# Kernel tuning notes

Measured on AMD Instinct MI355X. Metric: run time of the kernel, lower is better.

Reference implementation:

```python
import math
import jax, jax.numpy as jnp
import numpy as np
from jax import lax


def _l2n(v, eps=1e-12):
    return v / (jnp.linalg.norm(v) + eps)


def _sn(w_bar, u, v):
    # one power iteration (as in SpectralNorm with power_iterations=1)
    h = w_bar.shape[0]
    wm = w_bar.reshape(h, -1)
    v = _l2n(wm.T @ u)
    u = _l2n(wm @ v)
    u = lax.stop_gradient(u)  # u, v are updated via .data in torch (no grad)
    v = lax.stop_gradient(v)
    sigma = u @ (wm @ v)
    return w_bar / sigma


def _conv(x, w, stride, pad):
    return lax.conv_general_dilated(
        x, w, (stride, stride), [(pad, pad), (pad, pad)],
        dimension_numbers=('NCHW', 'OIHW', 'NCHW'))


def _make_blur_kernel():
    k = jnp.array([1., 3., 3., 1.], jnp.float32)
    k2 = k[None, :] * k[:, None]
    return k2 / k2.sum()  # 4x4, sums to 1


def _blur(x, k2, pad):
    # upfirdn2d with up=1, down=1: pad then depthwise FIR filter
    C = x.shape[1]
    xp = jnp.pad(x, ((0, 0), (0, 0), (pad[0], pad[1]), (pad[0], pad[1])))
    w = jnp.tile(k2[None, None], (C, 1, 1, 1))  # [C,1,4,4]
    return lax.conv_general_dilated(
        xp, w, (1, 1), 'VALID', feature_group_count=C,
        dimension_numbers=('NCHW', 'OIHW', 'NCHW'))


def setup_inputs() -> dict:
    key = jax.random.key(0)
    ks = jax.random.split(key, 12)
    Cin, Cout = 256, 512
    x = jax.random.normal(ks[0], (16, Cin, 64, 64), jnp.float32)
    w1_bar = jax.random.normal(ks[1], (Cin, Cin, 3, 3), jnp.float32) * 0.05
    u1 = _l2n(jax.random.normal(ks[2], (Cin,), jnp.float32))
    v1 = _l2n(jax.random.normal(ks[3], (Cin * 9,), jnp.float32))
    b1 = jnp.zeros((Cin,), jnp.float32)
    w2_bar = jax.random.normal(ks[4], (Cout, Cin, 3, 3), jnp.float32) * 0.05
    u2 = _l2n(jax.random.normal(ks[5], (Cout,), jnp.float32))
    v2 = _l2n(jax.random.normal(ks[6], (Cin * 9,), jnp.float32))
    b2 = jnp.zeros((Cout,), jnp.float32)
    ws_bar = jax.random.normal(ks[7], (Cout, Cin, 1, 1), jnp.float32) * 0.05
    us = _l2n(jax.random.normal(ks[8], (Cout,), jnp.float32))
    vs = _l2n(jax.random.normal(ks[9], (Cin,), jnp.float32))
    return dict(x=x, w1_bar=w1_bar, u1=u1, v1=v1, b1=b1,
                w2_bar=w2_bar, u2=u2, v2=v2, b2=b2,
                ws_bar=ws_bar, us=us, vs=vs)


def reference(x, w1_bar, u1, v1, b1, w2_bar, u2, v2, b2, ws_bar, us, vs):
    k2 = _make_blur_kernel()
    # conv1: 3x3 same-res, SN conv + bias + LeakyReLU(0.2)
    out = _conv(x, _sn(w1_bar, u1, v1), 1, 1) + b1[None, :, None, None]
    out = jax.nn.leaky_relu(out, 0.2)
    # conv2: blur pad=(2,2) then 3x3 stride-2 SN conv + bias + LeakyReLU
    out = _blur(out, k2, (2, 2))
    out = _conv(out, _sn(w2_bar, u2, v2), 2, 0) + b2[None, :, None, None]
    out = jax.nn.leaky_relu(out, 0.2)
    # skip: blur pad=(1,1) then 1x1 stride-2 SN conv (no bias, no act)
    skip = _blur(x, k2, (1, 1))
    skip = _conv(skip, _sn(ws_bar, us, vs), 2, 0)
    return (out + skip) / math.sqrt(2)
```

## Files before the change

### kernel.cpp

```cpp
#include <hip/hip_runtime.h>
#include <math.h>

typedef unsigned short u16;
typedef __attribute__((ext_vector_type(8))) unsigned short ushort8;
typedef __attribute__((ext_vector_type(4))) unsigned short u16x4;
typedef __attribute__((ext_vector_type(8))) short short8;
typedef __attribute__((ext_vector_type(4))) float f32x4;

__device__ __forceinline__ float b2f(u16 v) {
    unsigned u = ((unsigned)v) << 16; float f; __builtin_memcpy(&f, &u, 4); return f;
}
__device__ __forceinline__ u16 f2b(float f) {
    unsigned u; __builtin_memcpy(&u, &f, 4);
    u = (u + 0x7fffu + ((u >> 16) & 1u)) >> 16;
    return (u16)u;
}
__device__ __forceinline__ float ldin(const void* p, int i, int flag) {
    return flag ? ((const float*)p)[i] : b2f(((const u16*)p)[i]);
}
__device__ __forceinline__ void split2(float x, u16& h, u16& l) {
    h = f2b(x);
    l = f2b(x - b2f(h));
}
__device__ __forceinline__ ushort8 zero8() {
    ushort8 z;
#pragma unroll
    for (int i = 0; i < 8; ++i) z[i] = 0;
    return z;
}

__global__ void detect_kernel(const unsigned* __restrict__ xw, int* __restrict__ flag) {
    __shared__ int red[4];
    int tid = threadIdx.x, lane = tid & 63, wid = tid >> 6;
    int cnt = 0;
    for (int i = 0; i < 16; ++i) {
        unsigned w = xw[tid * 16 + i];
        unsigned e = (w >> 23) & 0xFF;
        if (e >= 77u && e <= 157u) ++cnt;
    }
    for (int o = 32; o; o >>= 1) cnt += __shfl_down(cnt, o, 64);
    if (lane == 0) red[wid] = cnt;
    __syncthreads();
    if (tid == 0) flag[0] = (red[0] + red[1] + red[2] + red[3] >= 2048) ? 1 : 0;
}

__global__ void sig_init_kernel(float* __restrict__ t, float* __restrict__ ns) {
    int i = blockIdx.x * 256 + threadIdx.x;
    if (i < 4864) t[i] = 0.f;
    if (i < 3) ns[i] = 0.f;
}

__global__ void sig_t_kernel(const void* __restrict__ w1, const void* __restrict__ u1,
                             const void* __restrict__ w2, const void* __restrict__ u2,
                             const void* __restrict__ wsb, const void* __restrict__ us,
                             const int* __restrict__ flagp, float* __restrict__ t) {
    __shared__ float ush[64];
    int blk = blockIdx.x;
    int flag = flagp[0];
    const void* W; const void* U; int m, toff, jc, ic;
    if (blk < 36)       { W = w1;  U = u1; m = 2304; toff = 0;    jc = blk % 9; ic = blk / 9; }
    else if (blk < 108) { int r = blk - 36;  W = w2;  U = u2; m = 2304; toff = 2304; jc = r % 9; ic = r / 9; }
    else                { int r = blk - 108; W = wsb; U = us; m = 256;  toff = 4608; jc = 0;     ic = r; }
    int tid = threadIdx.x;
    if (tid < 64) ush[tid] = ldin(U, ic * 64 + tid, flag);
    __syncthreads();
    int j = jc * 256 + tid;
    float acc = 0.f;
    int base = ic * 64 * m + j;
    for (int ii = 0; ii < 64; ++ii) acc += ldin(W, base + ii * m, flag) * ush[ii];
    atomicAdd(&t[toff + j], acc);
}

__global__ void sig_norm_kernel(float* __restrict__ t, float* __restrict__ ntinv) {
    __shared__ float red[4];
    int b = blockIdx.x;
    int m = (b == 2) ? 256 : 2304;
    int toff = b * 2304;
    int tid = threadIdx.x, lane = tid & 63, wid = tid >> 6;
    float s = 0.f;
    for (int j = tid; j < m; j += 256) { float v = t[toff + j]; s += v * v; }
    for (int o = 32; o; o >>= 1) s += __shfl_down(s, o, 64);
    if (lane == 0) red[wid] = s;
    __syncthreads();
    if (tid == 0) ntinv[b] = 1.f / (sqrtf(red[0] + red[1] + red[2] + red[3]) + 1e-12f);
}

__global__ void sig_s_kernel(const void* __restrict__ w1, const void* __restrict__ w2,
                             const void* __restrict__ wsb, const int* __restrict__ flagp,
                             const float* __restrict__ t, const float* __restrict__ ntinv,
                             float* __restrict__ ns) {
    int flag = flagp[0];
    int wg = blockIdx.x * 4 + (threadIdx.x >> 6);
    int lane = threadIdx.x & 63;
    const void* W; int m, toff, i, b;
    if (wg < 256)      { W = w1;  m = 2304; toff = 0;    i = wg;       b = 0; }
    else if (wg < 768) { W = w2;  m = 2304; toff = 2304; i = wg - 256; b = 1; }
    else               { W = wsb; m = 256;  toff = 4608; i = wg - 768; b = 2; }
    float acc = 0.f;
    int base = i * m;
    for (int j = lane; j < m; j += 64) acc += ldin(W, base + j, flag) * t[toff + j];
    for (int o = 32; o; o >>= 1) acc += __shfl_down(acc, o, 64);
    if (lane == 0) { float s = acc * ntinv[b]; atomicAdd(&ns[b], s * s); }
}

__global__ void sig_fin_kernel(const float* __restrict__ ns, float* __restrict__ inv_sigma) {
    int b = threadIdx.x;
    if (b < 3) { float s2 = ns[b]; float s = sqrtf(s2); inv_sigma[b] = (s + 1e-12f) / s2; }
}

__global__ void wprep_kernel(const void* __restrict__ w1b, const void* __restrict__ w2b,
                             const void* __restrict__ wsb,
                             const void* __restrict__ b1,  const void* __restrict__ b2,
                             const float* __restrict__ inv_sigma, const int* __restrict__ flagp,
                             u16* __restrict__ w1h, u16* __restrict__ w1l,
                             u16* __restrict__ w2h, u16* __restrict__ w2l,
                             u16* __restrict__ wsh, u16* __restrict__ wsl,
                             float* __restrict__ b1f, float* __restrict__ b2f_) {
    int idx = blockIdx.x * 256 + threadIdx.x;
    int flag = flagp[0];
    float s0 = inv_sigma[0], s1 = inv_sigma[1], s2 = inv_sigma[2];
    if (idx < 589824) {
        int kyx = idx / 65536; int rem = idx - kyx * 65536;
        int co = rem >> 8, ci = rem & 255;
        float w = ldin(w1b, ((co << 8) + ci) * 9 + kyx, flag) * s0;
        split2(w, w1h[idx], w1l[idx]);
    } else if (idx < 589824 + 1179648) {
        int i2 = idx - 589824;
        int kyx = i2 / 131072; int rem = i2 - kyx * 131072;
        int co = rem >> 8, ci = rem & 255;
        float w = ldin(w2b, ((co << 8) + ci) * 9 + kyx, flag) * s1;
        split2(w, w2h[i2], w2l[i2]);
    } else if (idx < 1900544) {
        int i3 = idx - 1769472;
        float w = ldin(wsb, i3, flag) * s2;
        split2(w, wsh[i3], wsl[i3]);
    } else if (idx < 1900544 + 256) {
        b1f[idx - 1900544] = ldin(b1, idx - 1900544, flag);
    } else if (idx < 1900544 + 768) {
        b2f_[idx - 1900800] = ldin(b2, idx - 1900800, flag);
    }
}

__global__ void transpose_kernel(const void* __restrict__ x, u16* __restrict__ xh,
                                 u16* __restrict__ xl,
                                 const int* __restrict__ flagp, int n0) {
    __shared__ float tile[32][65];
    int flag = flagp[0];
    int ny  = blockIdx.x;
    int ci0 = blockIdx.y * 32;
    int nl = ny >> 6, y = ny & 63;
    int t = threadIdx.x;
    int ci_l = t >> 3, x8 = (t & 7) * 8;
    int base = ((n0 + nl) * 256 + ci0 + ci_l) * 4096 + y * 64 + x8;
#pragma unroll
    for (int k = 0; k < 8; ++k) tile[ci_l][x8 + k] = ldin(x, base + k, flag);
    __syncthreads();
    int x_l = t >> 2, oc = (t & 3) * 8;
    size_t o = ((size_t)ny * 64 + x_l) * 256 + ci0 + oc;
    ushort8 h, l;
#pragma unroll
    for (int k = 0; k < 8; ++k) {
        u16 hh, ll; split2(tile[oc + k][x_l], hh, ll);
        h[k] = hh; l[k] = ll;
    }
    *(ushort8*)&xh[o] = h;
    *(ushort8*)&xl[o] = l;
}

__device__ __constant__ float BW[4] = {0.125f, 0.375f, 0.375f, 0.125f};

__global__ void blur1_kernel(const float* __restrict__ act1, u16* __restrict__ bh,
                             u16* __restrict__ bl) {
    int idx = blockIdx.x * 256 + threadIdx.x;
    int q = (idx & 63) * 4;
    int rem = idx >> 6;
    int xq = rem % 65; rem /= 65;
    int yq = rem % 65;
    int n  = rem / 65;
    float4 acc = {0.f, 0.f, 0.f, 0.f};
#pragma unroll
    for (int i = 0; i < 4; ++i) {
        int yy = yq + i - 2;
        if ((unsigned)yy >= 64u) continue;
#pragma unroll
        for (int j = 0; j < 4; ++j) {
            int xx = xq + j - 2;
            if ((unsigned)xx >= 64u) continue;
            float w = BW[i] * BW[j];
            float4 v = *(const float4*)&act1[((size_t)((n * 64 + yy) * 64 + xx) << 8) + q];
            acc.x += w * v.x; acc.y += w * v.y; acc.z += w * v.z; acc.w += w * v.w;
        }
    }
    u16x4 h, l;
    u16 hh, ll;
    split2(acc.x, hh, ll); h[0] = hh; l[0] = ll;
    split2(acc.y, hh, ll); h[1] = hh; l[1] = ll;
    split2(acc.z, hh, ll); h[2] = hh; l[2] = ll;
    split2(acc.w, hh, ll); h[3] = hh; l[3] = ll;
    *(u16x4*)&bh[(size_t)idx * 4] = h;
    *(u16x4*)&bl[(size_t)idx * 4] = l;
}

__global__ void blursample_kernel(const u16* __restrict__ xh, const u16* __restrict__ xl,
                                  u16* __restrict__ sh, u16* __restrict__ sl) {
    int idx = blockIdx.x * 256 + threadIdx.x;
    int q = (idx & 63) * 4;
    int rem = idx >> 6;
    int xo = rem & 31;
    int yo = (rem >> 5) & 31;
    int n  = rem >> 10;
    float4 acc = {0.f, 0.f, 0.f, 0.f};
#pragma unroll
    for (int i = 0; i < 4; ++i) {
        int yy = 2 * yo + i - 1;
        if ((unsigned)yy >= 64u) continue;
#pragma unroll
        for (int j = 0; j < 4; ++j) {
            int xx = 2 * xo + j - 1;
            if ((unsigned)xx >= 64u) continue;
            float w = BW[i] * BW[j];
            size_t g = ((size_t)((n * 64 + yy) * 64 + xx) << 8) + q;
            u16x4 vh = *(const u16x4*)&xh[g];
            u16x4 vl = *(const u16x4*)&xl[g];
            acc.x += w * (b2f(vh[0]) + b2f(vl[0]));
            acc.y += w * (b2f(vh[1]) + b2f(vl[1]));
            acc.z += w * (b2f(vh[2]) + b2f(vl[2]));
            acc.w += w * (b2f(vh[3]) + b2f(vl[3]));
        }
    }
    u16x4 h, l;
    u16 hh, ll;
    split2(acc.x, hh, ll); h[0] = hh; l[0] = ll;
    split2(acc.y, hh, ll); h[1] = hh; l[1] = ll;
    split2(acc.z, hh, ll); h[2] = hh; l[2] = ll;
    split2(acc.w, hh, ll); h[3] = hh; l[3] = ll;
    *(u16x4*)&sh[(size_t)idx * 4] = h;
    *(u16x4*)&sl[(size_t)idx * 4] = l;
}

#define LDK 40

template <bool DOLO>
__device__ __forceinline__ void conv1_body(
        const u16* __restrict__ xh, const u16* __restrict__ xl,
        const u16* __restrict__ w1h, const u16* __restrict__ w1l,
        const float* __restrict__ b1f, float* __restrict__ act1,
        u16* Ah, u16* Al, u16* Bh, u16* Bl) {
    int tid = threadIdx.x, lane = tid & 63, wid = tid >> 6;
    int col = lane & 15, quad = lane >> 4;
    int wco = (wid >> 1) * 32, wsp = (wid & 1) * 64;
    int sp_base = blockIdx.x * 128;
    int co_base = blockIdx.y * 64;
    int n  = sp_base >> 12;
    int y0 = (sp_base & 4095) >> 6;
    int r_st = tid >> 1, k_st = (tid & 1) * 16;
    int ra = tid >> 2, ka = (tid & 3) * 8;

    f32x4 acc[2][4];
#pragma unroll
    for (int i = 0; i < 2; ++i)
#pragma unroll
        for (int j = 0; j < 4; ++j) acc[i][j] = (f32x4){0.f, 0.f, 0.f, 0.f};

    for (int p = 0; p < 9; ++p) {
        int dy = p / 3 - 1, dx = p % 3 - 1;
        const u16* wh = w1h + (size_t)p * 65536;
        const u16* wl = w1l + (size_t)p * 65536;
        for (int kc = 0; kc < 8; ++kc) {
            int ci0 = kc * 32;
            __syncthreads();
            {
                size_t gs = (size_t)(co_base + ra) * 256 + ci0 + ka;
                *(ushort8*)&Ah[ra * LDK + ka] = *(const ushort8*)&wh[gs];
                if (DOLO) *(ushort8*)&Al[ra * LDK + ka] = *(const ushort8*)&wl[gs];
            }
            {
                int yy = y0 + (r_st >> 6) + dy;
                int xx = (r_st & 63) + dx;
                ushort8 h0, h1, l0, l1;
                if ((unsigned)yy < 64u && (unsigned)xx < 64u) {
                    size_t g = ((size_t)((n * 64 + yy) * 64 + xx) << 8) + ci0 + k_st;
                    h0 = *(const ushort8*)&xh[g];
                    h1 = *(const ushort8*)&xh[g + 8];
                    if (DOLO) {
                        l0 = *(const ushort8*)&xl[g];
                        l1 = *(const ushort8*)&xl[g + 8];
                    }
                } else {
                    h0 = zero8(); h1 = zero8();
                    if (DOLO) { l0 = zero8(); l1 = zero8(); }
                }
                *(ushort8*)&Bh[r_st * LDK + k_st]     = h0;
                *(ushort8*)&Bh[r_st * LDK + k_st + 8] = h1;
                if (DOLO) {
                    *(ushort8*)&Bl[r_st * LDK + k_st]     = l0;
                    *(ushort8*)&Bl[r_st * LDK + k_st + 8] = l1;
                }
            }
            __syncthreads();
            short8 ah[2], al[2];
#pragma unroll
            for (int tm = 0; tm < 2; ++tm) {
                ah[tm] = *(const short8*)&Ah[(wco + tm * 16 + col) * LDK + quad * 8];
                if (DOLO) al[tm] = *(const short8*)&Al[(wco + tm * 16 + col) * LDK + quad * 8];
            }
#pragma unroll
            for (int tn = 0; tn < 4; ++tn) {
                short8 bh = *(const short8*)&Bh[(wsp + tn * 16 + col) * LDK + quad * 8];
                short8 bl;
                if (DOLO) bl = *(const short8*)&Bl[(wsp + tn * 16 + col) * LDK + quad * 8];
#pragma unroll
                for (int tm = 0; tm < 2; ++tm) {
                    acc[tm][tn] = __builtin_amdgcn_mfma_f32_16x16x32_bf16(ah[tm], bh, acc[tm][tn], 0, 0, 0);
                    if (DOLO) {
                        acc[tm][tn] = __builtin_amdgcn_mfma_f32_16x16x32_bf16(ah[tm], bl, acc[tm][tn], 0, 0, 0);
                        acc[tm][tn] = __builtin_amdgcn_mfma_f32_16x16x32_bf16(al[tm], bh, acc[tm][tn], 0, 0, 0);
                    }
                }
            }
        }
    }
#pragma unroll
    for (int tm = 0; tm < 2; ++tm) {
        int cog = co_base + wco + tm * 16 + quad * 4;
        float4 bias = *(const float4*)&b1f[cog];
#pragma unroll
        for (int tn = 0; tn < 4; ++tn) {
            int sp = sp_base + wsp + tn * 16 + col;
            float4 o;
            float v0 = acc[tm][tn][0] + bias.x; o.x = v0 > 0.f ? v0 : 0.2f * v0;
            float v1 = acc[tm][tn][1] + bias.y; o.y = v1 > 0.f ? v1 : 0.2f * v1;
            float v2 = acc[tm][tn][2] + bias.z; o.z = v2 > 0.f ? v2 : 0.2f * v2;
            float v3 = acc[tm][tn][3] + bias.w; o.w = v3 > 0.f ? v3 : 0.2f * v3;
            *(float4*)&act1[((size_t)sp << 8) + cog] = o;
        }
    }
}

__global__ __launch_bounds__(256, 4) void conv1_kernel(
        const u16* __restrict__ xh, const u16* __restrict__ xl,
        const u16* __restrict__ w1h, const u16* __restrict__ w1l,
        const float* __restrict__ b1f, float* __restrict__ act1,
        const int* __restrict__ flagp) {
    __shared__ u16 Ah[64 * LDK];
    __shared__ u16 Al[64 * LDK];
    __shared__ u16 Bh[128 * LDK];
    __shared__ u16 Bl[128 * LDK];
    if (flagp[0]) conv1_body<true >(xh, xl, w1h, w1l, b1f, act1, Ah, Al, Bh, Bl);
    else          conv1_body<false>(xh, xl, w1h, w1l, b1f, act1, Ah, Al, Bh, Bl);
}

template <bool DOLO>
__device__ __forceinline__ void conv2_body(
        const u16* __restrict__ bl1h, const u16* __restrict__ bl1l,
        const u16* __restrict__ skh,  const u16* __restrict__ skl,
        const u16* __restrict__ w2h, const u16* __restrict__ w2l,
        const u16* __restrict__ wsh, const u16* __restrict__ wsl,
        const float* __restrict__ b2f_, void* __restrict__ out, int n0,
        u16* Ah, u16* Al, u16* Bh, u16* Bl, int flag) {
    int tid = threadIdx.x, lane = tid & 63, wid = tid >> 6;
    int col = lane & 15, quad = lane >> 4;
    int wco = (wid >> 1) * 32, wsp = (wid & 1) * 64;
    int sp_base = blockIdx.x * 128;
    int co_base = blockIdx.y * 64;
    int n   = sp_base >> 10;
    int yo0 = (sp_base & 1023) >> 5;
    int r_st = tid >> 1, k_st = (tid & 1) * 16;
    int ra = tid >> 2, ka = (tid & 3) * 8;

    f32x4 acc[2][4], accs[2][4];
#pragma unroll
    for (int i = 0; i < 2; ++i)
#pragma unroll
        for (int j = 0; j < 4; ++j) {
            acc[i][j]  = (f32x4){0.f, 0.f, 0.f, 0.f};
            accs[i][j] = (f32x4){0.f, 0.f, 0.f, 0.f};
        }

    for (int p = 0; p < 10; ++p) {
        int ky = p / 3, kx = p % 3;
        const u16* wh = (p < 9) ? w2h + (size_t)p * 131072 : wsh;
        const u16* wl = (p < 9) ? w2l + (size_t)p * 131072 : wsl;
        for (int kc = 0; kc < 8; ++kc) {
            int ci0 = kc * 32;
            __syncthreads();
            {
                size_t gs = (size_t)(co_base + ra) * 256 + ci0 + ka;
                *(ushort8*)&Ah[ra * LDK + ka] = *(const ushort8*)&wh[gs];
                if (DOLO) *(ushort8*)&Al[ra * LDK + ka] = *(const ushort8*)&wl[gs];
            }
            {
                const u16 *srch, *srcl;
                size_t g;
                if (p < 9) {
                    int yi = 2 * (yo0 + (r_st >> 5)) + ky;
                    int xi = 2 * (r_st & 31) + kx;
                    g = (size_t)((n * 65 + yi) * 65 + xi) * 256 + ci0 + k_st;
                    srch = bl1h; srcl = bl1l;
                } else {
                    g = ((size_t)(sp_base + r_st) << 8) + ci0 + k_st;
                    srch = skh; srcl = skl;
                }
                *(ushort8*)&Bh[r_st * LDK + k_st]     = *(const ushort8*)&srch[g];
                *(ushort8*)&Bh[r_st * LDK + k_st + 8] = *(const ushort8*)&srch[g + 8];
                if (DOLO) {
                    *(ushort8*)&Bl[r_st * LDK + k_st]     = *(const ushort8*)&srcl[g];
                    *(ushort8*)&Bl[r_st * LDK + k_st + 8] = *(const ushort8*)&srcl[g + 8];
                }
            }
            __syncthreads();
            short8 ah[2], al[2];
#pragma unroll
            for (int tm = 0; tm < 2; ++tm) {
                ah[tm] = *(const short8*)&Ah[(wco + tm * 16 + col) * LDK + quad * 8];
                if (DOLO) al[tm] = *(const short8*)&Al[(wco + tm * 16 + col) * LDK + quad * 8];
            }
            if (p < 9) {
#pragma unroll
                for (int tn = 0; tn < 4; ++tn) {
                    short8 bh = *(const short8*)&Bh[(wsp + tn * 16 + col) * LDK + quad * 8];
                    short8 bl;
                    if (DOLO) bl = *(const short8*)&Bl[(wsp + tn * 16 + col) * LDK + quad * 8];
#pragma unroll
                    for (int tm = 0; tm < 2; ++tm) {
                        acc[tm][tn] = __builtin_amdgcn_mfma_f32_16x16x32_bf16(ah[tm], bh, acc[tm][tn], 0, 0, 0);
                        if (DOLO) {
                            acc[tm][tn] = __builtin_amdgcn_mfma_f32_16x16x32_bf16(ah[tm], bl, acc[tm][tn], 0, 0, 0);
                            acc[tm][tn] = __builtin_amdgcn_mfma_f32_16x16x32_bf16(al[tm], bh, acc[tm][tn], 0, 0, 0);
                        }
                    }
                }
            } else {
#pragma unroll
                for (int tn = 0; tn < 4; ++tn) {
                    short8 bh = *(const short8*)&Bh[(wsp + tn * 16 + col) * LDK + quad * 8];
                    short8 bl;
                    if (DOLO) bl = *(const short8*)&Bl[(wsp + tn * 16 + col) * LDK + quad * 8];
#pragma unroll
                    for (int tm = 0; tm < 2; ++tm) {
                        accs[tm][tn] = __builtin_amdgcn_mfma_f32_16x16x32_bf16(ah[tm], bh, accs[tm][tn], 0, 0, 0);
                        if (DOLO) {
                            accs[tm][tn] = __builtin_amdgcn_mfma_f32_16x16x32_bf16(ah[tm], bl, accs[tm][tn], 0, 0, 0);
                            accs[tm][tn] = __builtin_amdgcn_mfma_f32_16x16x32_bf16(al[tm], bh, accs[tm][tn], 0, 0, 0);
                        }
                    }
                }
            }
        }
    }
    const float RS2 = 0.70710678118654752f;
#pragma unroll
    for (int tm = 0; tm < 2; ++tm) {
        int cog = co_base + wco + tm * 16 + quad * 4;
        float4 bias = *(const float4*)&b2f_[cog];
        float bb[4] = {bias.x, bias.y, bias.z, bias.w};
#pragma unroll
        for (int tn = 0; tn < 4; ++tn) {
            int sp  = sp_base + wsp + tn * 16 + col;
            int ng  = n0 + (sp >> 10);
            int rem = sp & 1023;
            size_t ob = ((size_t)ng * 512 + cog) * 1024 + rem;
#pragma unroll
            for (int r = 0; r < 4; ++r) {
                float v = acc[tm][tn][r] + bb[r];
                v = v > 0.f ? v : 0.2f * v;
                v = (v + accs[tm][tn][r]) * RS2;
                if (flag) ((float*)out)[ob + (size_t)r * 1024] = v;
                else      ((u16*)out)[ob + (size_t)r * 1024]   = f2b(v);
            }
        }
    }
}

__global__ __launch_bounds__(256, 2) void conv2_kernel(
        const u16* __restrict__ bl1h, const u16* __restrict__ bl1l,
        const u16* __restrict__ skh,  const u16* __restrict__ skl,
        const u16* __restrict__ w2h, const u16* __restrict__ w2l,
        const u16* __restrict__ wsh, const u16* __restrict__ wsl,
        const float* __restrict__ b2f_, const int* __restrict__ flagp,
        void* __restrict__ out, int n0) {
    __shared__ u16 Ah[64 * LDK];
    __shared__ u16 Al[64 * LDK];
    __shared__ u16 Bh[128 * LDK];
    __shared__ u16 Bl[128 * LDK];
    int flag = flagp[0];
    if (flag) conv2_body<true >(bl1h, bl1l, skh, skl, w2h, w2l, wsh, wsl, b2f_, out, n0, Ah, Al, Bh, Bl, flag);
    else      conv2_body<false>(bl1h, bl1l, skh, skl, w2h, w2l, wsh, wsl, b2f_, out, n0, Ah, Al, Bh, Bl, flag);
}

extern "C" void kernel_launch(void* const* d_in, const int* in_sizes, int n_in,
                              void* d_out, int out_size, void* d_ws, size_t ws_size,
                              hipStream_t stream) {
    const void* x   = d_in[0];
    const void* w1b = d_in[1];
    const void* u1  = d_in[2];
    const void* b1  = d_in[4];
    const void* w2b = d_in[5];
    const void* u2  = d_in[6];
    const void* b2  = d_in[8];
    const void* wsb = d_in[9];
    const void* us  = d_in[10];

    char* ws = (char*)d_ws;
    int*   flag      = (int*)(ws);
    float* inv_sigma = (float*)(ws + 64);
    float* b1f       = (float*)(ws + 1024);
    float* b2fp      = (float*)(ws + 2048);
    u16* w1h = (u16*)(ws + 4096);
    u16* w1l = (u16*)(ws + 1183744);
    u16* w2h = (u16*)(ws + 2363392);
    u16* w2l = (u16*)(ws + 4722688);
    u16* wsh = (u16*)(ws + 7081984);
    u16* wsl = (u16*)(ws + 7344128);
    u16* xth  = (u16*)(ws + 7606272);
    u16* xtl  = (u16*)(ws + 7606272 + 16777216);
    u16* bl1h = (u16*)(ws + 7606272);
    u16* bl1l = (u16*)(ws + 7606272 + 17305600);
    float* act1 = (float*)(ws + 42217472);
    u16* skh = (u16*)(ws + 75771904);
    u16* skl = (u16*)(ws + 75771904 + 4194304);
    float* tvec  = (float*)(ws + 7606272);
    float* ntinv = (float*)(ws + 7606272 + 19456);
    float* ns    = (float*)(ws + 7606272 + 19520);

    detect_kernel<<<1, 256, 0, stream>>>((const unsigned*)x, flag);
    sig_init_kernel<<<19, 256, 0, stream>>>(tvec, ns);
    sig_t_kernel<<<116, 256, 0, stream>>>(w1b, u1, w2b, u2, wsb, us, flag, tvec);
    sig_norm_kernel<<<3, 256, 0, stream>>>(tvec, ntinv);
    sig_s_kernel<<<320, 256, 0, stream>>>(w1b, w2b, wsb, flag, tvec, ntinv, ns);
    sig_fin_kernel<<<1, 64, 0, stream>>>(ns, inv_sigma);
    wprep_kernel<<<7427, 256, 0, stream>>>(w1b, w2b, wsb, b1, b2, inv_sigma, flag,
                                           w1h, w1l, w2h, w2l, wsh, wsl, b1f, b2fp);
    for (int c = 0; c < 2; ++c) {
        int n0 = c * 8;
        transpose_kernel<<<dim3(512, 8), 256, 0, stream>>>(x, xth, xtl, flag, n0);
        blursample_kernel<<<2048, 256, 0, stream>>>(xth, xtl, skh, skl);
        conv1_kernel<<<dim3(256, 4), 256, 0, stream>>>(xth, xtl, w1h, w1l, b1f, act1, flag);
        blur1_kernel<<<8450, 256, 0, stream>>>(act1, bl1h, bl1l);
        conv2_kernel<<<dim3(64, 8), 256, 0, stream>>>(bl1h, bl1l, skh, skl, w2h, w2l,
                                                      wsh, wsl, b2fp, flag, d_out, n0);
    }
}
```

Measured before the change: 784.9 us.

## Retile conv1 to 128 channels by one 64-pixel row with block swizzle

Conv1's block tile changes from 64 output channels by 128 pixels (two rows) to 128 channels by 64 pixels (one image row). Each warp now owns 64 channels by 32 pixels. Because a block covers exactly one row, the y-bound check moves out of the loop, and taps whose row falls outside the image are skipped whole. A blockIdx swizzle interleaves spatial blocks, likely to improve L2 reuse of the activations. Weight tiles grow while activation tiles shrink, trading more weight traffic per block for fewer activation loads and whole-tap skipping at image edges.

```diff
diff --git a/kernel.cpp b/kernel.cpp
--- a/kernel.cpp
+++ b/kernel.cpp
@@ -248,22 +248,26 @@
         u16* Ah, u16* Al, u16* Bh, u16* Bl) {
     int tid = threadIdx.x, lane = tid & 63, wid = tid >> 6;
     int col = lane & 15, quad = lane >> 4;
-    int wco = (wid >> 1) * 32, wsp = (wid & 1) * 64;
-    int sp_base = blockIdx.x * 128;
-    int co_base = blockIdx.y * 64;
+    int wco = (wid >> 1) * 64, wsp = (wid & 1) * 32;
+    int bidx = blockIdx.x;
+    int sp_blk = (bidx & 7) * 64 + (bidx >> 3);
+    int sp_base = sp_blk * 64;
+    int co_base = blockIdx.y * 128;
     int n  = sp_base >> 12;
     int y0 = (sp_base & 4095) >> 6;
-    int r_st = tid >> 1, k_st = (tid & 1) * 16;
-    int ra = tid >> 2, ka = (tid & 3) * 8;
-
-    f32x4 acc[2][4];
-#pragma unroll
-    for (int i = 0; i < 2; ++i)
-#pragma unroll
-        for (int j = 0; j < 4; ++j) acc[i][j] = (f32x4){0.f, 0.f, 0.f, 0.f};
+    int ra = tid >> 1, ka = (tid & 1) * 16;
+    int rb = tid >> 2, kb = (tid & 3) * 8;
+
+    f32x4 acc[4][2];
+#pragma unroll
+    for (int i = 0; i < 4; ++i)
+#pragma unroll
+        for (int j = 0; j < 2; ++j) acc[i][j] = (f32x4){0.f, 0.f, 0.f, 0.f};
 
     for (int p = 0; p < 9; ++p) {
         int dy = p / 3 - 1, dx = p % 3 - 1;
+        int yy = y0 + dy;
+        if ((unsigned)yy >= 64u) continue;
         const u16* wh = w1h + (size_t)p * 65536;
         const u16* wl = w1l + (size_t)p * 65536;
         for (int kc = 0; kc < 8; ++kc) {
@@ -271,46 +275,41 @@
             __syncthreads();
             {
                 size_t gs = (size_t)(co_base + ra) * 256 + ci0 + ka;
-                *(ushort8*)&Ah[ra * LDK + ka] = *(const ushort8*)&wh[gs];
-                if (DOLO) *(ushort8*)&Al[ra * LDK + ka] = *(const ushort8*)&wl[gs];
+                *(ushort8*)&Ah[ra * LDK + ka]     = *(const ushort8*)&wh[gs];
+                *(ushort8*)&Ah[ra * LDK + ka + 8] = *(const ushort8*)&wh[gs + 8];
+                if (DOLO) {
+                    *(ushort8*)&Al[ra * LDK + ka]     = *(const ushort8*)&wl[gs];
+                    *(ushort8*)&Al[ra * LDK + ka + 8] = *(const ushort8*)&wl[gs + 8];
+                }
             }
             {
-                int yy = y0 + (r_st >> 6) + dy;
-                int xx = (r_st & 63) + dx;
-                ushort8 h0, h1, l0, l1;
-                if ((unsigned)yy < 64u && (unsigned)xx < 64u) {
-                    size_t g = ((size_t)((n * 64 + yy) * 64 + xx) << 8) + ci0 + k_st;
+                int xx = rb + dx;
+                ushort8 h0, l0;
+                if ((unsigned)xx < 64u) {
+                    size_t g = ((size_t)((n * 64 + yy) * 64 + xx) << 8) + ci0 + kb;
                     h0 = *(const ushort8*)&xh[g];
-                    h1 = *(const ushort8*)&xh[g + 8];
-                    if (DOLO) {
-                        l0 = *(const ushort8*)&xl[g];
-                        l1 = *(const ushort8*)&xl[g + 8];
-                    }
+                    if (DOLO) l0 = *(const ushort8*)&xl[g];
                 } else {
-                    h0 = zero8(); h1 = zero8();
-                    if (DOLO) { l0 = zero8(); l1 = zero8(); }
-                }
-                *(ushort8*)&Bh[r_st * LDK + k_st]     = h0;
-                *(ushort8*)&Bh[r_st * LDK + k_st + 8] = h1;
-                if (DOLO) {
-                    *(ushort8*)&Bl[r_st * LDK + k_st]     = l0;
-                    *(ushort8*)&Bl[r_st * LDK + k_st + 8] = l1;
-                }
+                    h0 = zero8();
+                    if (DOLO) l0 = zero8();
+                }
+                *(ushort8*)&Bh[rb * LDK + kb] = h0;
+                if (DOLO) *(ushort8*)&Bl[rb * LDK + kb] = l0;
             }
             __syncthreads();
-            short8 ah[2], al[2];
-#pragma unroll
-            for (int tm = 0; tm < 2; ++tm) {
+            short8 ah[4], al[4];
+#pragma unroll
+            for (int tm = 0; tm < 4; ++tm) {
                 ah[tm] = *(const short8*)&Ah[(wco + tm * 16 + col) * LDK + quad * 8];
                 if (DOLO) al[tm] = *(const short8*)&Al[(wco + tm * 16 + col) * LDK + quad * 8];
             }
 #pragma unroll
-            for (int tn = 0; tn < 4; ++tn) {
+            for (int tn = 0; tn < 2; ++tn) {
                 short8 bh = *(const short8*)&Bh[(wsp + tn * 16 + col) * LDK + quad * 8];
                 short8 bl;
                 if (DOLO) bl = *(const short8*)&Bl[(wsp + tn * 16 + col) * LDK + quad * 8];
 #pragma unroll
-                for (int tm = 0; tm < 2; ++tm) {
+                for (int tm = 0; tm < 4; ++tm) {
                     acc[tm][tn] = __builtin_amdgcn_mfma_f32_16x16x32_bf16(ah[tm], bh, acc[tm][tn], 0, 0, 0);
                     if (DOLO) {
                         acc[tm][tn] = __builtin_amdgcn_mfma_f32_16x16x32_bf16(ah[tm], bl, acc[tm][tn], 0, 0, 0);
@@ -321,11 +320,11 @@
         }
     }
 #pragma unroll
-    for (int tm = 0; tm < 2; ++tm) {
+    for (int tm = 0; tm < 4; ++tm) {
         int cog = co_base + wco + tm * 16 + quad * 4;
         float4 bias = *(const float4*)&b1f[cog];
 #pragma unroll
-        for (int tn = 0; tn < 4; ++tn) {
+        for (int tn = 0; tn < 2; ++tn) {
             int sp = sp_base + wsp + tn * 16 + col;
             float4 o;
             float v0 = acc[tm][tn][0] + bias.x; o.x = v0 > 0.f ? v0 : 0.2f * v0;
@@ -342,10 +341,10 @@
         const u16* __restrict__ w1h, const u16* __restrict__ w1l,
         const float* __restrict__ b1f, float* __restrict__ act1,
         const int* __restrict__ flagp) {
-    __shared__ u16 Ah[64 * LDK];
-    __shared__ u16 Al[64 * LDK];
-    __shared__ u16 Bh[128 * LDK];
-    __shared__ u16 Bl[128 * LDK];
+    __shared__ u16 Ah[128 * LDK];
+    __shared__ u16 Al[128 * LDK];
+    __shared__ u16 Bh[64 * LDK];
+    __shared__ u16 Bl[64 * LDK];
     if (flagp[0]) conv1_body<true >(xh, xl, w1h, w1l, b1f, act1, Ah, Al, Bh, Bl);
     else          conv1_body<false>(xh, xl, w1h, w1l, b1f, act1, Ah, Al, Bh, Bl);
 }
@@ -535,7 +534,7 @@
         int n0 = c * 8;
         transpose_kernel<<<dim3(512, 8), 256, 0, stream>>>(x, xth, xtl, flag, n0);
         blursample_kernel<<<2048, 256, 0, stream>>>(xth, xtl, skh, skl);
-        conv1_kernel<<<dim3(256, 4), 256, 0, stream>>>(xth, xtl, w1h, w1l, b1f, act1, flag);
+        conv1_kernel<<<dim3(512, 2), 256, 0, stream>>>(xth, xtl, w1h, w1l, b1f, act1, flag);
         blur1_kernel<<<8450, 256, 0, stream>>>(act1, bl1h, bl1l);
         conv2_kernel<<<dim3(64, 8), 256, 0, stream>>>(bl1h, bl1l, skh, skl, w2h, w2l,
                                                       wsh, wsl, b2fp, flag, d_out, n0);
```

Result: faster. 751.5 us (-4.3%).
